# Kernel tuning notes

Measured on AMD Instinct MI355X. Metric: run time of the kernel, lower is better.

Reference implementation:

```python
import jax, jax.numpy as jnp
import numpy as np

B, CH, H, W = 16, 4, 512, 512
HIDDEN = 8

def _filters():
    ident = jnp.array([[0.,0.,0.],[0.,1.,0.],[0.,0.,0.]])
    sobel_x = jnp.array([[-1.,0.,1.],[-2.,0.,2.],[-1.,0.,1.]])
    sobel_y = sobel_x.T
    lap = jnp.array([[1.,2.,1.],[2.,-12.,2.],[1.,2.,1.]])
    return jnp.stack([ident, sobel_x, sobel_y, lap])  # [4,3,3]

def setup_inputs() -> dict:
    key = jax.random.key(0)
    k1, k2, k3, k4, k5 = jax.random.split(key, 5)
    return {
        "x": jax.random.normal(k1, (B, CH, H, W), dtype=jnp.float32),
        "w1_w": jax.random.normal(k2, (HIDDEN, 4 * CH), dtype=jnp.float32) * 0.1,
        "w1_b": jax.random.normal(k3, (HIDDEN,), dtype=jnp.float32) * 0.1,
        "w2_w": jax.random.normal(k4, (CH, HIDDEN), dtype=jnp.float32) * 0.1,
        "noise": jax.random.uniform(k5, (B, 1, H, W), dtype=jnp.float32),
    }

def reference(x, w1_w, w1_b, w2_w, noise):
    filters = _filters()  # fixed (non-learned) perception kernels
    b, ch, h, w = x.shape
    # circular pad + per-channel (depthwise, 4 filters per channel) 3x3 conv
    xp = jnp.pad(x, ((0, 0), (0, 0), (1, 1), (1, 1)), mode="wrap")
    y = jax.lax.conv_general_dilated(
        xp.reshape(b * ch, 1, h + 2, w + 2),
        filters[:, None],  # [4,1,3,3]
        window_strides=(1, 1), padding="VALID",
        dimension_numbers=("NCHW", "OIHW", "NCHW"),
    ).reshape(b, ch * 4, h, w)  # channel order: (ch, filter)
    # 1x1 conv MLP: 16 -> 8 (relu) -> 4
    hdn = jax.nn.relu(jnp.einsum("bchw,oc->bohw", y, w1_w) + w1_b[None, :, None, None])
    dx = jnp.einsum("bchw,oc->bohw", hdn, w2_w)
    # stochastic update mask: floor(U[0,1) + update_rate), update_rate=0.5
    mask = jnp.floor(noise + 0.5)
    return x + dx * mask
```

## Files before the change

kernel.cpp:

```cpp
#include <hip/hip_runtime.h>
#include <math.h>

namespace {
constexpr int B  = 16;
constexpr int CH = 4;
constexpr int H  = 512;
constexpr int W  = 512;
constexpr int HID = 8;

__global__ __launch_bounds__(256) void ca_kernel(
    const float* __restrict__ x,
    const float* __restrict__ w1w,
    const float* __restrict__ w1b,
    const float* __restrict__ w2w,
    const float* __restrict__ noise,
    float* __restrict__ out)
{
    const int idx = blockIdx.x * 256 + threadIdx.x;
    const int w4 = idx & (W / 4 - 1);
    const int h  = (idx >> 7) & (H - 1);
    const int b  = idx >> 16;

    const int w0 = w4 << 2;
    const int wl = (w0 - 1) & (W - 1);
    const int wr = (w0 + 4) & (W - 1);
    const int hm = (h - 1) & (H - 1);
    const int hp = (h + 1) & (H - 1);

    float hpre[HID][4];
#pragma unroll
    for (int o = 0; o < HID; ++o) {
        const float bo = w1b[o];
#pragma unroll
        for (int j = 0; j < 4; ++j) hpre[o][j] = bo;
    }

    float xc[CH][4];

#pragma unroll
    for (int c = 0; c < CH; ++c) {
        const float* base = x + (size_t)(b * CH + c) * (H * W);
        const float* rt = base + hm * W;
        const float* rc = base + h  * W;
        const float* rb = base + hp * W;
        const float4 t4 = *(const float4*)(rt + w0);
        const float4 c4 = *(const float4*)(rc + w0);
        const float4 b4 = *(const float4*)(rb + w0);
        const float t[6]  = { rt[wl], t4.x, t4.y, t4.z, t4.w, rt[wr] };
        const float mm[6] = { rc[wl], c4.x, c4.y, c4.z, c4.w, rc[wr] };
        const float bb[6] = { rb[wl], b4.x, b4.y, b4.z, b4.w, rb[wr] };
        xc[c][0] = c4.x; xc[c][1] = c4.y; xc[c][2] = c4.z; xc[c][3] = c4.w;

#pragma unroll
        for (int j = 0; j < 4; ++j) {
            const float a00 = t[j],  a01 = t[j+1],  a02 = t[j+2];
            const float a10 = mm[j], a11 = mm[j+1], a12 = mm[j+2];
            const float a20 = bb[j], a21 = bb[j+1], a22 = bb[j+2];
            const float id = a11;
            const float sx = (a02 - a00) + 2.f * (a12 - a10) + (a22 - a20);
            const float sy = (a20 - a00) + 2.f * (a21 - a01) + (a22 - a02);
            const float lp = (a00 + a02 + a20 + a22)
                           + 2.f * (a01 + a10 + a12 + a21) - 12.f * a11;
#pragma unroll
            for (int o = 0; o < HID; ++o) {
                const float* wr1 = w1w + o * 16 + c * 4;
                hpre[o][j] = fmaf(id, wr1[0],
                             fmaf(sx, wr1[1],
                             fmaf(sy, wr1[2],
                             fmaf(lp, wr1[3], hpre[o][j]))));
            }
        }
    }

    const float4 nz = *(const float4*)(noise + ((size_t)b * H + h) * W + w0);
    const float msk[4] = { floorf(nz.x + 0.5f), floorf(nz.y + 0.5f),
                           floorf(nz.z + 0.5f), floorf(nz.w + 0.5f) };

#pragma unroll
    for (int o = 0; o < HID; ++o)
#pragma unroll
        for (int j = 0; j < 4; ++j)
            hpre[o][j] = fmaxf(hpre[o][j], 0.f);

#pragma unroll
    for (int c = 0; c < CH; ++c) {
        float d[4] = { 0.f, 0.f, 0.f, 0.f };
#pragma unroll
        for (int o = 0; o < HID; ++o) {
            const float wv = w2w[c * HID + o];
#pragma unroll
            for (int j = 0; j < 4; ++j) d[j] = fmaf(hpre[o][j], wv, d[j]);
        }
        float4 ov;
        ov.x = fmaf(d[0], msk[0], xc[c][0]);
        ov.y = fmaf(d[1], msk[1], xc[c][1]);
        ov.z = fmaf(d[2], msk[2], xc[c][2]);
        ov.w = fmaf(d[3], msk[3], xc[c][3]);
        *(float4*)(out + ((size_t)(b * CH + c) * H + h) * W + w0) = ov;
    }
}
}

extern "C" void kernel_launch(void* const* d_in, const int* in_sizes, int n_in,
                              void* d_out, int out_size, void* d_ws, size_t ws_size,
                              hipStream_t stream) {
    const float* x     = (const float*)d_in[0];
    const float* w1w   = (const float*)d_in[1];
    const float* w1b   = (const float*)d_in[2];
    const float* w2w   = (const float*)d_in[3];
    const float* noise = (const float*)d_in[4];
    float* out = (float*)d_out;

    const int total_threads = B * H * (W / 4);
    ca_kernel<<<total_threads / 256, 256, 0, stream>>>(x, w1w, w1b, w2w, noise, out);
}
```

Measured before the change: 43.20 us.

## Process eight pixels per thread with packed FP32 FMAs and separable stencil

Each thread now handles 8 horizontal pixels instead of 4, which halves the thread count and amortizes halo loads. The 1x1 MLP arithmetic moves to two-wide float vectors so the compiler can emit packed FP32 FMA instructions. The Sobel and Laplacian filters are rebuilt from shared column sums and differences to cut ALU work. The costs are higher register pressure and lower occupancy, which could hurt latency hiding in this memory-bound kernel.

Result: slower. 45.77 us (+5.9%).

```diff
diff --git a/kernel.cpp b/kernel.cpp
--- a/kernel.cpp
+++ b/kernel.cpp
@@ -2,11 +2,16 @@
 #include <math.h>
 
 namespace {
-constexpr int B  = 16;
-constexpr int CH = 4;
-constexpr int H  = 512;
-constexpr int W  = 512;
+typedef float v2f __attribute__((ext_vector_type(2)));
+
+constexpr int B   = 16;
+constexpr int CH  = 4;
+constexpr int H   = 512;
+constexpr int W   = 512;
 constexpr int HID = 8;
+constexpr int PX  = 8;
+
+static __device__ __forceinline__ v2f splat(float f) { v2f r; r.x = f; r.y = f; return r; }
 
 __global__ __launch_bounds__(256) void ca_kernel(
     const float* __restrict__ x,
@@ -17,25 +22,25 @@
     float* __restrict__ out)
 {
     const int idx = blockIdx.x * 256 + threadIdx.x;
-    const int w4 = idx & (W / 4 - 1);
-    const int h  = (idx >> 7) & (H - 1);
-    const int b  = idx >> 16;
+    const int wg = idx & (W / PX - 1);
+    const int h  = (idx >> 6) & (H - 1);
+    const int b  = idx >> 15;
 
-    const int w0 = w4 << 2;
+    const int w0 = wg << 3;
     const int wl = (w0 - 1) & (W - 1);
-    const int wr = (w0 + 4) & (W - 1);
+    const int wr = (w0 + PX) & (W - 1);
     const int hm = (h - 1) & (H - 1);
     const int hp = (h + 1) & (H - 1);
 
-    float hpre[HID][4];
+    v2f hpre[HID][4];
 #pragma unroll
     for (int o = 0; o < HID; ++o) {
-        const float bo = w1b[o];
+        const v2f bo = splat(w1b[o]);
 #pragma unroll
-        for (int j = 0; j < 4; ++j) hpre[o][j] = bo;
+        for (int p = 0; p < 4; ++p) hpre[o][p] = bo;
     }
 
-    float xc[CH][4];
+    v2f xc[CH][4];
 
 #pragma unroll
     for (int c = 0; c < CH; ++c) {
@@ -43,60 +48,96 @@
         const float* rt = base + hm * W;
         const float* rc = base + h  * W;
         const float* rb = base + hp * W;
-        const float4 t4 = *(const float4*)(rt + w0);
-        const float4 c4 = *(const float4*)(rc + w0);
-        const float4 b4 = *(const float4*)(rb + w0);
-        const float t[6]  = { rt[wl], t4.x, t4.y, t4.z, t4.w, rt[wr] };
-        const float mm[6] = { rc[wl], c4.x, c4.y, c4.z, c4.w, rc[wr] };
-        const float bb[6] = { rb[wl], b4.x, b4.y, b4.z, b4.w, rb[wr] };
-        xc[c][0] = c4.x; xc[c][1] = c4.y; xc[c][2] = c4.z; xc[c][3] = c4.w;
+
+        float t[10], m[10], bt[10];
+        {
+            const float4 a = *(const float4*)(rt + w0);
+            const float4 q = *(const float4*)(rt + w0 + 4);
+            t[0] = rt[wl]; t[1] = a.x; t[2] = a.y; t[3] = a.z; t[4] = a.w;
+            t[5] = q.x; t[6] = q.y; t[7] = q.z; t[8] = q.w; t[9] = rt[wr];
+        }
+        {
+            const float4 a = *(const float4*)(rc + w0);
+            const float4 q = *(const float4*)(rc + w0 + 4);
+            m[0] = rc[wl]; m[1] = a.x; m[2] = a.y; m[3] = a.z; m[4] = a.w;
+            m[5] = q.x; m[6] = q.y; m[7] = q.z; m[8] = q.w; m[9] = rc[wr];
+        }
+        {
+            const float4 a = *(const float4*)(rb + w0);
+            const float4 q = *(const float4*)(rb + w0 + 4);
+            bt[0] = rb[wl]; bt[1] = a.x; bt[2] = a.y; bt[3] = a.z; bt[4] = a.w;
+            bt[5] = q.x; bt[6] = q.y; bt[7] = q.z; bt[8] = q.w; bt[9] = rb[wr];
+        }
+
+        float s[10], d[10];
+#pragma unroll
+        for (int k = 0; k < 10; ++k) {
+            s[k] = fmaf(2.f, m[k], t[k] + bt[k]);
+            d[k] = bt[k] - t[k];
+        }
 
 #pragma unroll
-        for (int j = 0; j < 4; ++j) {
-            const float a00 = t[j],  a01 = t[j+1],  a02 = t[j+2];
-            const float a10 = mm[j], a11 = mm[j+1], a12 = mm[j+2];
-            const float a20 = bb[j], a21 = bb[j+1], a22 = bb[j+2];
-            const float id = a11;
-            const float sx = (a02 - a00) + 2.f * (a12 - a10) + (a22 - a20);
-            const float sy = (a20 - a00) + 2.f * (a21 - a01) + (a22 - a02);
-            const float lp = (a00 + a02 + a20 + a22)
-                           + 2.f * (a01 + a10 + a12 + a21) - 12.f * a11;
+        for (int p = 0; p < 4; ++p) {
+            const int j0 = 2 * p, j1 = 2 * p + 1;
+            v2f id, sx, sy, lp;
+            id.x = m[j0 + 1];                      id.y = m[j1 + 1];
+            sx.x = s[j0 + 2] - s[j0];              sx.y = s[j1 + 2] - s[j1];
+            sy.x = fmaf(2.f, d[j0 + 1], d[j0] + d[j0 + 2]);
+            sy.y = fmaf(2.f, d[j1 + 1], d[j1] + d[j1 + 2]);
+            lp.x = fmaf(-16.f, m[j0 + 1], fmaf(2.f, s[j0 + 1], s[j0] + s[j0 + 2]));
+            lp.y = fmaf(-16.f, m[j1 + 1], fmaf(2.f, s[j1 + 1], s[j1] + s[j1 + 2]));
+
+            xc[c][p] = id;
+
 #pragma unroll
             for (int o = 0; o < HID; ++o) {
-                const float* wr1 = w1w + o * 16 + c * 4;
-                hpre[o][j] = fmaf(id, wr1[0],
-                             fmaf(sx, wr1[1],
-                             fmaf(sy, wr1[2],
-                             fmaf(lp, wr1[3], hpre[o][j]))));
+                const float* w1r = w1w + o * 16 + c * 4;
+                v2f acc = hpre[o][p];
+                acc = __builtin_elementwise_fma(id, splat(w1r[0]), acc);
+                acc = __builtin_elementwise_fma(sx, splat(w1r[1]), acc);
+                acc = __builtin_elementwise_fma(sy, splat(w1r[2]), acc);
+                acc = __builtin_elementwise_fma(lp, splat(w1r[3]), acc);
+                hpre[o][p] = acc;
             }
         }
     }
 
-    const float4 nz = *(const float4*)(noise + ((size_t)b * H + h) * W + w0);
-    const float msk[4] = { floorf(nz.x + 0.5f), floorf(nz.y + 0.5f),
-                           floorf(nz.z + 0.5f), floorf(nz.w + 0.5f) };
+    const float* nrow = noise + ((size_t)b * H + h) * W + w0;
+    const float4 n0 = *(const float4*)(nrow);
+    const float4 n1 = *(const float4*)(nrow + 4);
+    v2f msk[4];
+    msk[0].x = floorf(n0.x + 0.5f); msk[0].y = floorf(n0.y + 0.5f);
+    msk[1].x = floorf(n0.z + 0.5f); msk[1].y = floorf(n0.w + 0.5f);
+    msk[2].x = floorf(n1.x + 0.5f); msk[2].y = floorf(n1.y + 0.5f);
+    msk[3].x = floorf(n1.z + 0.5f); msk[3].y = floorf(n1.w + 0.5f);
 
 #pragma unroll
     for (int o = 0; o < HID; ++o)
 #pragma unroll
-        for (int j = 0; j < 4; ++j)
-            hpre[o][j] = fmaxf(hpre[o][j], 0.f);
+        for (int p = 0; p < 4; ++p)
+            hpre[o][p] = __builtin_elementwise_max(hpre[o][p], splat(0.f));
 
 #pragma unroll
     for (int c = 0; c < CH; ++c) {
-        float d[4] = { 0.f, 0.f, 0.f, 0.f };
+        v2f dd[4] = { splat(0.f), splat(0.f), splat(0.f), splat(0.f) };
 #pragma unroll
         for (int o = 0; o < HID; ++o) {
-            const float wv = w2w[c * HID + o];
+            const v2f wv = splat(w2w[c * HID + o]);
 #pragma unroll
-            for (int j = 0; j < 4; ++j) d[j] = fmaf(hpre[o][j], wv, d[j]);
+            for (int p = 0; p < 4; ++p)
+                dd[p] = __builtin_elementwise_fma(hpre[o][p], wv, dd[p]);
         }
-        float4 ov;
-        ov.x = fmaf(d[0], msk[0], xc[c][0]);
-        ov.y = fmaf(d[1], msk[1], xc[c][1]);
-        ov.z = fmaf(d[2], msk[2], xc[c][2]);
-        ov.w = fmaf(d[3], msk[3], xc[c][3]);
-        *(float4*)(out + ((size_t)(b * CH + c) * H + h) * W + w0) = ov;
+        v2f ov[4];
+#pragma unroll
+        for (int p = 0; p < 4; ++p)
+            ov[p] = __builtin_elementwise_fma(dd[p], msk[p], xc[c][p]);
+
+        float* orow = out + ((size_t)(b * CH + c) * H + h) * W + w0;
+        float4 o0, o1;
+        o0.x = ov[0].x; o0.y = ov[0].y; o0.z = ov[1].x; o0.w = ov[1].y;
+        o1.x = ov[2].x; o1.y = ov[2].y; o1.z = ov[3].x; o1.w = ov[3].y;
+        *(float4*)(orow)     = o0;
+        *(float4*)(orow + 4) = o1;
     }
 }
 }
@@ -111,6 +152,6 @@
     const float* noise = (const float*)d_in[4];
     float* out = (float*)d_out;
 
-    const int total_threads = B * H * (W / 4);
+    const int total_threads = B * H * (W / PX);
     ca_kernel<<<total_threads / 256, 256, 0, stream>>>(x, w1w, w1b, w2w, noise, out);
 }
```

## Stream row strips through LDS ring buffer with async global-to-LDS loads

Applied to the files above, without the earlier changes.

Each block processes an 8-row strip of one batch image. Input rows for all channels are loaded with asynchronous global_load_lds into a 5-slot LDS ring, and the wait counters are set so the next row's fetch overlaps compute on the current one. Stencil partial sums are shared between neighbouring columns and computed with packed 2-wide FMAs. This cuts redundant global and L2 reads of neighbour rows, at the cost of large LDS usage per block, fewer blocks in flight, halo re-reads at strip edges, and fragile manual vmcnt accounting.

Measured after the change: 35.75 us. -17.3%, faster.

```diff
diff --git a/kernel.cpp b/kernel.cpp
--- a/kernel.cpp
+++ b/kernel.cpp
@@ -2,11 +2,14 @@
 #include <math.h>
 
 namespace {
-constexpr int B  = 16;
-constexpr int CH = 4;
-constexpr int H  = 512;
-constexpr int W  = 512;
-constexpr int HID = 8;
+typedef float v2f __attribute__((ext_vector_type(2)));
+
+constexpr int B = 16, CH = 4, H = 512, W = 512, HID = 8;
+constexpr int STRIP  = 8;
+constexpr int SLOT_F = CH * W;
+constexpr int NSLOT  = 5;
+
+static __device__ __forceinline__ v2f splat(float f){ v2f r; r.x=f; r.y=f; return r; }
 
 __global__ __launch_bounds__(256) void ca_kernel(
     const float* __restrict__ x,
@@ -16,87 +19,118 @@
     const float* __restrict__ noise,
     float* __restrict__ out)
 {
-    const int idx = blockIdx.x * 256 + threadIdx.x;
-    const int w4 = idx & (W / 4 - 1);
-    const int h  = (idx >> 7) & (H - 1);
-    const int b  = idx >> 16;
+    __shared__ float smem[NSLOT * SLOT_F];
 
-    const int w0 = w4 << 2;
-    const int wl = (w0 - 1) & (W - 1);
-    const int wr = (w0 + 4) & (W - 1);
-    const int hm = (h - 1) & (H - 1);
-    const int hp = (h + 1) & (H - 1);
+    const int blk  = blockIdx.x;
+    const int b    = blk >> 6;
+    const int hs   = (blk & 63) * STRIP;
+    const int tid  = threadIdx.x;
+    const int wv   = tid >> 6;
+    const int lane = tid & 63;
+    const int w0   = tid << 1;
+    const int colL = (w0 - 1) & (W - 1);
+    const int colR = (w0 + 2) & (W - 1);
 
-    float hpre[HID][4];
+    const float* xb = x + (size_t)b * CH * H * W;
+
+    auto dma = [&](int q, int slot) {
+        const int row  = q & (H - 1);
+        const int half = wv & 1;
 #pragma unroll
-    for (int o = 0; o < HID; ++o) {
-        const float bo = w1b[o];
+        for (int j = 0; j < 2; ++j) {
+            const int ch = (wv >> 1) + 2 * j;
+            const float* g = xb + ((size_t)ch * H + row) * W + half * 256 + lane * 4;
+            const float* l = &smem[slot * SLOT_F + ch * W + half * 256];
+            __builtin_amdgcn_global_load_lds(
+                (const __attribute__((address_space(1))) void*)g,
+                (__attribute__((address_space(3))) void*)l, 16, 0, 0);
+        }
+    };
+
+    dma(hs - 1, 0); dma(hs, 1); dma(hs + 1, 2);
+    asm volatile("" ::: "memory");
+    dma(hs + 2, 3);
+
+    int sA = 0, sB = 1, sC = 2, sW = 4;
+
+    for (int i = 0; i < STRIP; ++i) {
+        const int r = hs + i;
+        if (i == 0)              asm volatile("s_waitcnt vmcnt(2)" ::: "memory");
+        else if (i == STRIP - 1) asm volatile("s_waitcnt vmcnt(5)" ::: "memory");
+        else                     asm volatile("s_waitcnt vmcnt(7)" ::: "memory");
+        __builtin_amdgcn_s_barrier();
+        if (i + 3 <= STRIP) dma(r + 3, sW);
+
+        v2f hpre[HID];
 #pragma unroll
-        for (int j = 0; j < 4; ++j) hpre[o][j] = bo;
-    }
-
-    float xc[CH][4];
+        for (int o = 0; o < HID; ++o) hpre[o] = splat(w1b[o]);
+        v2f xcv[CH];
 
 #pragma unroll
-    for (int c = 0; c < CH; ++c) {
-        const float* base = x + (size_t)(b * CH + c) * (H * W);
-        const float* rt = base + hm * W;
-        const float* rc = base + h  * W;
-        const float* rb = base + hp * W;
-        const float4 t4 = *(const float4*)(rt + w0);
-        const float4 c4 = *(const float4*)(rc + w0);
-        const float4 b4 = *(const float4*)(rb + w0);
-        const float t[6]  = { rt[wl], t4.x, t4.y, t4.z, t4.w, rt[wr] };
-        const float mm[6] = { rc[wl], c4.x, c4.y, c4.z, c4.w, rc[wr] };
-        const float bb[6] = { rb[wl], b4.x, b4.y, b4.z, b4.w, rb[wr] };
-        xc[c][0] = c4.x; xc[c][1] = c4.y; xc[c][2] = c4.z; xc[c][3] = c4.w;
+        for (int ch = 0; ch < CH; ++ch) {
+            const float* rT = &smem[sA * SLOT_F + ch * W];
+            const float* rM = &smem[sB * SLOT_F + ch * W];
+            const float* rB2 = &smem[sC * SLOT_F + ch * W];
+            const float2 t2 = *(const float2*)&rT[w0];
+            const float2 m2 = *(const float2*)&rM[w0];
+            const float2 b2 = *(const float2*)&rB2[w0];
+            const float tL = rT[colL], tR = rT[colR];
+            const float mL = rM[colL], mR = rM[colR];
+            const float bL = rB2[colL], bR = rB2[colR];
+
+            v2f tv; tv.x = t2.x; tv.y = t2.y;
+            v2f mv; mv.x = m2.x; mv.y = m2.y;
+            v2f bv; bv.x = b2.x; bv.y = b2.y;
+            const v2f sP = __builtin_elementwise_fma(splat(2.f), mv, tv + bv);
+            const v2f dP = bv - tv;
+            const float sL = fmaf(2.f, mL, tL + bL);
+            const float sR = fmaf(2.f, mR, tR + bR);
+            const float dL = bL - tL, dR = bR - tR;
+
+            v2f sprev; sprev.x = sL;   sprev.y = sP.x;
+            v2f snext; snext.x = sP.y; snext.y = sR;
+            v2f dprev; dprev.x = dL;   dprev.y = dP.x;
+            v2f dnext; dnext.x = dP.y; dnext.y = dR;
+
+            const v2f id = mv;
+            const v2f sx = snext - sprev;
+            const v2f sy = __builtin_elementwise_fma(splat(2.f), dP, dprev + dnext);
+            const v2f lp = __builtin_elementwise_fma(splat(-16.f), mv,
+                            __builtin_elementwise_fma(splat(2.f), sP, sprev + snext));
+            xcv[ch] = mv;
+#pragma unroll
+            for (int o = 0; o < HID; ++o) {
+                const float* w1r = w1w + o * 16 + ch * 4;
+                v2f a = hpre[o];
+                a = __builtin_elementwise_fma(id, splat(w1r[0]), a);
+                a = __builtin_elementwise_fma(sx, splat(w1r[1]), a);
+                a = __builtin_elementwise_fma(sy, splat(w1r[2]), a);
+                a = __builtin_elementwise_fma(lp, splat(w1r[3]), a);
+                hpre[o] = a;
+            }
+        }
 
 #pragma unroll
-        for (int j = 0; j < 4; ++j) {
-            const float a00 = t[j],  a01 = t[j+1],  a02 = t[j+2];
-            const float a10 = mm[j], a11 = mm[j+1], a12 = mm[j+2];
-            const float a20 = bb[j], a21 = bb[j+1], a22 = bb[j+2];
-            const float id = a11;
-            const float sx = (a02 - a00) + 2.f * (a12 - a10) + (a22 - a20);
-            const float sy = (a20 - a00) + 2.f * (a21 - a01) + (a22 - a02);
-            const float lp = (a00 + a02 + a20 + a22)
-                           + 2.f * (a01 + a10 + a12 + a21) - 12.f * a11;
-#pragma unroll
-            for (int o = 0; o < HID; ++o) {
-                const float* wr1 = w1w + o * 16 + c * 4;
-                hpre[o][j] = fmaf(id, wr1[0],
-                             fmaf(sx, wr1[1],
-                             fmaf(sy, wr1[2],
-                             fmaf(lp, wr1[3], hpre[o][j]))));
-            }
-        }
-    }
+        for (int o = 0; o < HID; ++o)
+            hpre[o] = __builtin_elementwise_max(hpre[o], splat(0.f));
 
-    const float4 nz = *(const float4*)(noise + ((size_t)b * H + h) * W + w0);
-    const float msk[4] = { floorf(nz.x + 0.5f), floorf(nz.y + 0.5f),
-                           floorf(nz.z + 0.5f), floorf(nz.w + 0.5f) };
+        const float2 nz = *(const float2*)&noise[((size_t)b * H + r) * W + w0];
+        v2f mk; mk.x = floorf(nz.x + 0.5f); mk.y = floorf(nz.y + 0.5f);
 
 #pragma unroll
-    for (int o = 0; o < HID; ++o)
+        for (int ch = 0; ch < CH; ++ch) {
+            v2f dd = splat(0.f);
 #pragma unroll
-        for (int j = 0; j < 4; ++j)
-            hpre[o][j] = fmaxf(hpre[o][j], 0.f);
+            for (int o = 0; o < HID; ++o)
+                dd = __builtin_elementwise_fma(hpre[o], splat(w2w[ch * HID + o]), dd);
+            const v2f ov = __builtin_elementwise_fma(dd, mk, xcv[ch]);
+            float2 st; st.x = ov.x; st.y = ov.y;
+            *(float2*)&out[((size_t)(b * CH + ch) * H + r) * W + w0] = st;
+        }
 
-#pragma unroll
-    for (int c = 0; c < CH; ++c) {
-        float d[4] = { 0.f, 0.f, 0.f, 0.f };
-#pragma unroll
-        for (int o = 0; o < HID; ++o) {
-            const float wv = w2w[c * HID + o];
-#pragma unroll
-            for (int j = 0; j < 4; ++j) d[j] = fmaf(hpre[o][j], wv, d[j]);
-        }
-        float4 ov;
-        ov.x = fmaf(d[0], msk[0], xc[c][0]);
-        ov.y = fmaf(d[1], msk[1], xc[c][1]);
-        ov.z = fmaf(d[2], msk[2], xc[c][2]);
-        ov.w = fmaf(d[3], msk[3], xc[c][3]);
-        *(float4*)(out + ((size_t)(b * CH + c) * H + h) * W + w0) = ov;
+        sA = sB; sB = sC;
+        sC = (sC + 1 == NSLOT) ? 0 : sC + 1;
+        sW = (sW + 1 == NSLOT) ? 0 : sW + 1;
     }
 }
 }
@@ -111,6 +145,6 @@
     const float* noise = (const float*)d_in[4];
     float* out = (float*)d_out;
 
-    const int total_threads = B * H * (W / 4);
-    ca_kernel<<<total_threads / 256, 256, 0, stream>>>(x, w1w, w1b, w2w, noise, out);
+    const int blocks = B * (H / STRIP);
+    ca_kernel<<<blocks, 256, 0, stream>>>(x, w1w, w1b, w2w, noise, out);
 }
```
